# Optimization experiments

Hardware: AMD Instinct MI355X
Metric: run time of the kernel (lower is better)

The kernel has to match this reference:

```python
import jax, jax.numpy as jnp
import numpy as np

N, E, F, T, H = 100000, 3_200_000, 64, 12, 32


def _lin(k, fin, fout):
    s = 1.0 / np.sqrt(fin)
    k1, k2 = jax.random.split(k)
    W = jax.random.uniform(k1, (fin, fout), jnp.float32, -s, s)
    b = jax.random.uniform(k2, (fout,), jnp.float32, -s, s)
    return W, b


def _lstm_w(k, fin):
    s = 1.0 / np.sqrt(H)
    k1, k2, k3, k4 = jax.random.split(k, 4)
    return (jax.random.uniform(k1, (4 * H, fin), jnp.float32, -s, s),
            jax.random.uniform(k2, (4 * H, H), jnp.float32, -s, s),
            jax.random.uniform(k3, (4 * H,), jnp.float32, -s, s),
            jax.random.uniform(k4, (4 * H,), jnp.float32, -s, s))


def setup_inputs() -> dict:
    key = jax.random.key(0)
    ks = jax.random.split(key, 12)
    x = jax.random.normal(ks[0], (N, F), jnp.float32)
    edge_index = jax.random.randint(ks[1], (2, E), 0, N, dtype=jnp.int32)
    W_fp, b_fp = _lin(ks[2], F, 64)
    W_g1, b_g1 = _lin(ks[3], 64, 64)
    W_g2, b_g2 = _lin(ks[4], 64, 32)
    W_g3, b_g3 = _lin(ks[5], 32, 16)
    W_tp, b_tp = _lin(ks[6], 1, 16)
    Wih0, Whh0, bih0, bhh0 = _lstm_w(ks[7], 16)
    Wih1, Whh1, bih1, bhh1 = _lstm_w(ks[8], H)
    W_fc1, b_fc1 = _lin(ks[9], H, 16)
    W_fc2, b_fc2 = _lin(ks[10], 16, 1)
    return dict(x=x, edge_index=edge_index, W_fp=W_fp, b_fp=b_fp,
                W_g1=W_g1, b_g1=b_g1, W_g2=W_g2, b_g2=b_g2, W_g3=W_g3, b_g3=b_g3,
                W_tp=W_tp, b_tp=b_tp,
                Wih0=Wih0, Whh0=Whh0, bih0=bih0, bhh0=bhh0,
                Wih1=Wih1, Whh1=Whh1, bih1=bih1, bhh1=bhh1,
                W_fc1=W_fc1, b_fc1=b_fc1, W_fc2=W_fc2, b_fc2=b_fc2)


def reference(x, edge_index, W_fp, b_fp, W_g1, b_g1, W_g2, b_g2, W_g3, b_g3,
              W_tp, b_tp, Wih0, Whh0, bih0, bhh0, Wih1, Whh1, bih1, bhh1,
              W_fc1, b_fc1, W_fc2, b_fc2):
    n = x.shape[0]
    loops = jnp.arange(n, dtype=edge_index.dtype)
    src = jnp.concatenate([edge_index[0], loops])  # self-loops, PyG GCNConv default
    dst = jnp.concatenate([edge_index[1], loops])
    deg = jax.ops.segment_sum(jnp.ones_like(src, dtype=x.dtype), dst, num_segments=n)
    dis = deg ** -0.5  # deg >= 1 because of self-loops
    norm = dis[src] * dis[dst]  # [E+N]

    def gcn(h, W, b):
        h = h @ W  # transform then propagate (PyG order)
        agg = jax.ops.segment_sum(h[src] * norm[:, None], dst, num_segments=n)
        return agg + b

    h = jax.nn.relu(x @ W_fp + b_fp)
    h = jax.nn.relu(gcn(h, W_g1, b_g1))        # dropout inactive (eval mode)
    h = jax.nn.relu(gcn(h, W_g2, b_g2))
    h_gcn = jax.nn.relu(gcn(h, W_g3, b_g3))    # NOTE: overwritten in original forward (dead)

    # temporal branch: last T raw features -> [N, T, 1] -> proj to 16
    t = x[:, -T:].reshape(n, T, 1) @ W_tp + b_tp  # [N, T, 16]

    def step(carry, xt):
        h0, c0, h1, c1 = carry
        g = xt @ Wih0.T + h0 @ Whh0.T + (bih0 + bhh0)
        i, f, gg, o = jnp.split(g, 4, axis=-1)  # torch gate order i,f,g,o
        c0 = jax.nn.sigmoid(f) * c0 + jax.nn.sigmoid(i) * jnp.tanh(gg)
        h0 = jax.nn.sigmoid(o) * jnp.tanh(c0)
        g = h0 @ Wih1.T + h1 @ Whh1.T + (bih1 + bhh1)
        i, f, gg, o = jnp.split(g, 4, axis=-1)
        c1 = jax.nn.sigmoid(f) * c1 + jax.nn.sigmoid(i) * jnp.tanh(gg)
        h1 = jax.nn.sigmoid(o) * jnp.tanh(c1)
        return (h0, c0, h1, c1), None

    z = jnp.zeros((n, H), x.dtype)
    (h0, c0, h1, c1), _ = jax.lax.scan(step, (z, z, z, z), jnp.swapaxes(t, 0, 1))
    out = jax.nn.relu(h1 @ W_fc1 + b_fc1) @ W_fc2 + b_fc2  # [N, 1]
    return out
```

## Files before the change

kernel.cpp:

```cpp
#include <hip/hip_runtime.h>


#define TSTEPS 12
#define BS 512
#define NPB (BS / 4)

__device__ __forceinline__ float fsig(float x) {
    float e = __expf(-x);
    return __builtin_amdgcn_rcpf(1.0f + e);
}

__device__ __forceinline__ float ftanh(float x) {
    float ax = fabsf(x);
    float e = __expf(-2.0f * ax);
    float r = (1.0f - e) * __builtin_amdgcn_rcpf(1.0f + e);
    return x < 0.0f ? -r : r;
}

__global__ void precomp_kernel(const float* __restrict__ Wih0,
                               const float* __restrict__ Wtp,
                               const float* __restrict__ btp,
                               const float* __restrict__ bih0,
                               const float* __restrict__ bhh0,
                               const float* __restrict__ bih1,
                               const float* __restrict__ bhh1,
                               float* __restrict__ ws) {
    int r = threadIdx.x;
    if (r < 128) {
        float a = 0.0f, c = 0.0f;
#pragma unroll
        for (int k = 0; k < 16; ++k) {
            float w = Wih0[r * 16 + k];
            a += w * Wtp[k];
            c += w * btp[k];
        }
        const int g4 = r >> 5;
        const int j  = r & 31;
        ws[j * 8 + g4]       = a;
        ws[j * 8 + 4 + g4]   = c + bih0[r] + bhh0[r];
        ws[256 + j * 4 + g4] = bih1[r] + bhh1[r];
    }
}

__device__ __forceinline__ float dot8(const float4 a0, const float4 a1,
                                      const float h[8]) {
    return a0.x*h[0] + a0.y*h[1] + a0.z*h[2] + a0.w*h[3]
         + a1.x*h[4] + a1.y*h[5] + a1.z*h[6] + a1.w*h[7];
}

__device__ __forceinline__ float rs4(float v0, float v1, float v2, float v3,
                                     bool hi2, bool hi1) {
    float sa = hi2 ? v0 : v2;
    float ka = hi2 ? v2 : v0;
    float sb = hi2 ? v1 : v3;
    float kb = hi2 ? v3 : v1;
    float u0 = ka + __shfl_xor(sa, 2);
    float u1 = kb + __shfl_xor(sb, 2);
    float sc = hi1 ? u0 : u1;
    float kc = hi1 ? u1 : u0;
    return kc + __shfl_xor(sc, 1);
}

__global__ __launch_bounds__(BS) void lstm_kernel(
    const float* __restrict__ x,
    const float* __restrict__ Whh0,
    const float* __restrict__ Wih1,
    const float* __restrict__ Whh1,
    const float* __restrict__ Wfc1,
    const float* __restrict__ bfc1,
    const float* __restrict__ Wfc2,
    const float* __restrict__ bfc2,
    const float* __restrict__ pre,
    float* __restrict__ out, int N)
{
    __shared__ __align__(16) float sW[12288];

    const int tid = threadIdx.x;
#pragma unroll
    for (int i = 0; i < 8; ++i) sW[i * BS + tid]        = Whh0[i * BS + tid];
#pragma unroll
    for (int i = 0; i < 8; ++i) sW[4096 + i * BS + tid] = Wih1[i * BS + tid];
#pragma unroll
    for (int i = 0; i < 8; ++i) sW[8192 + i * BS + tid] = Whh1[i * BS + tid];
    __syncthreads();

    const int s    = tid & 3;
    const int node = tid >> 2;
    const int so8  = s * 8;
    const bool hi2 = (s & 2) != 0;
    const bool hi1 = (s & 1) != 0;
    const int n  = blockIdx.x * NPB + node;
    const int nn = (n < N) ? n : (N > 0 ? N - 1 : 0);
    const float* xr = x + (size_t)nn * 64 + 52;

    float h0r[8], h1r[8], c0r[8], c1r[8], hn[8];
#pragma unroll
    for (int k = 0; k < 8; ++k) { h0r[k] = 0.0f; h1r[k] = 0.0f; c0r[k] = 0.0f; c1r[k] = 0.0f; }

#pragma unroll 1
    for (int t = 0; t < TSTEPS; ++t) {
        const float xval = xr[t];

#pragma unroll
        for (int jj = 0; jj < 8; ++jj) {
            const int jown = so8 + jj;
            float pI[4], pF[4], pG[4], pO[4];
#pragma unroll
            for (int g = 0; g < 4; ++g) {
                const int j = g * 8 + jj;
                const float* wi = &sW[(j      ) * 32 + so8];
                const float* wf = &sW[(j +  32) * 32 + so8];
                const float* wg = &sW[(j +  64) * 32 + so8];
                const float* wo = &sW[(j +  96) * 32 + so8];
                pI[g] = dot8(((const float4*)wi)[0], ((const float4*)wi)[1], h0r);
                pF[g] = dot8(((const float4*)wf)[0], ((const float4*)wf)[1], h0r);
                pG[g] = dot8(((const float4*)wg)[0], ((const float4*)wg)[1], h0r);
                pO[g] = dot8(((const float4*)wo)[0], ((const float4*)wo)[1], h0r);
                __builtin_amdgcn_sched_barrier(0);
            }
            const float SI = rs4(pI[0], pI[1], pI[2], pI[3], hi2, hi1);
            const float SF = rs4(pF[0], pF[1], pF[2], pF[3], hi2, hi1);
            const float SG = rs4(pG[0], pG[1], pG[2], pG[3], hi2, hi1);
            const float SO = rs4(pO[0], pO[1], pO[2], pO[3], hi2, hi1);
            const float4 pA = ((const float4*)pre)[jown * 2];
            const float4 pC = ((const float4*)pre)[jown * 2 + 1];
            const float gi = SI + pC.x + xval * pA.x;
            const float gf = SF + pC.y + xval * pA.y;
            const float gG = SG + pC.z + xval * pA.z;
            const float go = SO + pC.w + xval * pA.w;
            const float cc = fsig(gf) * c0r[jj] + fsig(gi) * ftanh(gG);
            c0r[jj] = cc;
            hn[jj]  = fsig(go) * ftanh(cc);
        }
#pragma unroll
        for (int k = 0; k < 8; ++k) h0r[k] = hn[k];

#pragma unroll
        for (int jj = 0; jj < 8; ++jj) {
            const int jown = so8 + jj;
            float pI[4], pF[4], pG[4], pO[4];
#pragma unroll
            for (int g = 0; g < 4; ++g) {
                const int j = g * 8 + jj;
                {
                    const float* ai = &sW[4096 + (j      ) * 32 + so8];
                    const float* af = &sW[4096 + (j +  32) * 32 + so8];
                    const float* ag = &sW[4096 + (j +  64) * 32 + so8];
                    const float* ao = &sW[4096 + (j +  96) * 32 + so8];
                    pI[g] = dot8(((const float4*)ai)[0], ((const float4*)ai)[1], h0r);
                    pF[g] = dot8(((const float4*)af)[0], ((const float4*)af)[1], h0r);
                    pG[g] = dot8(((const float4*)ag)[0], ((const float4*)ag)[1], h0r);
                    pO[g] = dot8(((const float4*)ao)[0], ((const float4*)ao)[1], h0r);
                }
                __builtin_amdgcn_sched_barrier(0);
                {
                    const float* bi = &sW[8192 + (j      ) * 32 + so8];
                    const float* bf = &sW[8192 + (j +  32) * 32 + so8];
                    const float* bg = &sW[8192 + (j +  64) * 32 + so8];
                    const float* bo = &sW[8192 + (j +  96) * 32 + so8];
                    pI[g] += dot8(((const float4*)bi)[0], ((const float4*)bi)[1], h1r);
                    pF[g] += dot8(((const float4*)bf)[0], ((const float4*)bf)[1], h1r);
                    pG[g] += dot8(((const float4*)bg)[0], ((const float4*)bg)[1], h1r);
                    pO[g] += dot8(((const float4*)bo)[0], ((const float4*)bo)[1], h1r);
                }
                __builtin_amdgcn_sched_barrier(0);
            }
            const float SI = rs4(pI[0], pI[1], pI[2], pI[3], hi2, hi1);
            const float SF = rs4(pF[0], pF[1], pF[2], pF[3], hi2, hi1);
            const float SG = rs4(pG[0], pG[1], pG[2], pG[3], hi2, hi1);
            const float SO = rs4(pO[0], pO[1], pO[2], pO[3], hi2, hi1);
            const float4 pD = ((const float4*)(pre + 256))[jown];
            const float gi = SI + pD.x;
            const float gf = SF + pD.y;
            const float gG = SG + pD.z;
            const float go = SO + pD.w;
            const float cc = fsig(gf) * c1r[jj] + fsig(gi) * ftanh(gG);
            c1r[jj] = cc;
            hn[jj]  = fsig(go) * ftanh(cc);
        }
#pragma unroll
        for (int k = 0; k < 8; ++k) h1r[k] = hn[k];
    }

    float am[16];
#pragma unroll
    for (int m = 0; m < 16; ++m) am[m] = 0.0f;
#pragma unroll 1
    for (int kk = 0; kk < 8; ++kk) {
        const float* row = Wfc1 + (size_t)(so8 + kk) * 16;
        const float4 r0 = ((const float4*)row)[0];
        const float4 r1 = ((const float4*)row)[1];
        const float4 r2 = ((const float4*)row)[2];
        const float4 r3 = ((const float4*)row)[3];
        const float hv = h1r[kk];
        am[ 0] += r0.x*hv; am[ 1] += r0.y*hv; am[ 2] += r0.z*hv; am[ 3] += r0.w*hv;
        am[ 4] += r1.x*hv; am[ 5] += r1.y*hv; am[ 6] += r1.z*hv; am[ 7] += r1.w*hv;
        am[ 8] += r2.x*hv; am[ 9] += r2.y*hv; am[10] += r2.z*hv; am[11] += r2.w*hv;
        am[12] += r3.x*hv; am[13] += r3.y*hv; am[14] += r3.z*hv; am[15] += r3.w*hv;
    }
    float acc = bfc2[0];
#pragma unroll
    for (int m = 0; m < 16; ++m) {
        float a = am[m];
        a += __shfl_xor(a, 1); a += __shfl_xor(a, 2);
        acc += fmaxf(a + bfc1[m], 0.0f) * Wfc2[m];
    }
    if (s == 0 && n < N) out[n] = acc;
}

extern "C" void kernel_launch(void* const* d_in, const int* in_sizes, int n_in,
                              void* d_out, int out_size, void* d_ws, size_t ws_size,
                              hipStream_t stream) {
    (void)n_in; (void)out_size; (void)ws_size;
    const float* x    = (const float*)d_in[0];
    const float* Wtp  = (const float*)d_in[10];
    const float* btp  = (const float*)d_in[11];
    const float* Wih0 = (const float*)d_in[12];
    const float* Whh0 = (const float*)d_in[13];
    const float* bih0 = (const float*)d_in[14];
    const float* bhh0 = (const float*)d_in[15];
    const float* Wih1 = (const float*)d_in[16];
    const float* Whh1 = (const float*)d_in[17];
    const float* bih1 = (const float*)d_in[18];
    const float* bhh1 = (const float*)d_in[19];
    const float* Wfc1 = (const float*)d_in[20];
    const float* bfc1 = (const float*)d_in[21];
    const float* Wfc2 = (const float*)d_in[22];
    const float* bfc2 = (const float*)d_in[23];

    float* out = (float*)d_out;
    float* pre = (float*)d_ws;

    const int N = in_sizes[0] / 64;

    precomp_kernel<<<1, 128, 0, stream>>>(Wih0, Wtp, btp, bih0, bhh0, bih1, bhh1, pre);
    lstm_kernel<<<(N + NPB - 1) / NPB, BS, 0, stream>>>(
        x, Whh0, Wih1, Whh1, Wfc1, bfc1, Wfc2, bfc2, pre, out, N);
}
```

Before: 1.262 ms.

## Spill LSTM cell state to LDS and regroup gate dot products

```diff
diff --git a/kernel.cpp b/kernel.cpp
--- a/kernel.cpp
+++ b/kernel.cpp
@@ -59,6 +59,47 @@
     float sc = hi1 ? u0 : u1;
     float kc = hi1 ? u1 : u0;
     return kc + __shfl_xor(sc, 1);
+}
+
+__device__ __forceinline__ void l0pair(const float* __restrict__ sW,
+                                       int jj, int so8, int offA, int offB,
+                                       const float h[8], bool hi2, bool hi1,
+                                       float& SA, float& SB) {
+    float4 a0[4], a1[4], b0[4], b1[4];
+#pragma unroll
+    for (int g = 0; g < 4; ++g) {
+        const float* wa = &sW[(g * 8 + jj + offA) * 32 + so8];
+        const float* wb = &sW[(g * 8 + jj + offB) * 32 + so8];
+        a0[g] = ((const float4*)wa)[0]; a1[g] = ((const float4*)wa)[1];
+        b0[g] = ((const float4*)wb)[0]; b1[g] = ((const float4*)wb)[1];
+    }
+    float pa[4], pb[4];
+#pragma unroll
+    for (int g = 0; g < 4; ++g) {
+        pa[g] = dot8(a0[g], a1[g], h);
+        pb[g] = dot8(b0[g], b1[g], h);
+    }
+    SA = rs4(pa[0], pa[1], pa[2], pa[3], hi2, hi1);
+    SB = rs4(pb[0], pb[1], pb[2], pb[3], hi2, hi1);
+}
+
+__device__ __forceinline__ float l1gate(const float* __restrict__ sW,
+                                        int jj, int so8, int off,
+                                        const float h0[8], const float h1[8],
+                                        bool hi2, bool hi1) {
+    float4 a0[4], a1[4], b0[4], b1[4];
+#pragma unroll
+    for (int g = 0; g < 4; ++g) {
+        const float* ax = &sW[4096 + (g * 8 + jj + off) * 32 + so8];
+        const float* bx = &sW[8192 + (g * 8 + jj + off) * 32 + so8];
+        a0[g] = ((const float4*)ax)[0]; a1[g] = ((const float4*)ax)[1];
+        b0[g] = ((const float4*)bx)[0]; b1[g] = ((const float4*)bx)[1];
+    }
+    float p[4];
+#pragma unroll
+    for (int g = 0; g < 4; ++g)
+        p[g] = dot8(a0[g], a1[g], h0) + dot8(b0[g], b1[g], h1);
+    return rs4(p[0], p[1], p[2], p[3], hi2, hi1);
 }
 
 __global__ __launch_bounds__(BS) void lstm_kernel(
@@ -74,6 +115,8 @@
     float* __restrict__ out, int N)
 {
     __shared__ __align__(16) float sW[12288];
+    __shared__ float sc0[8 * BS];
+    __shared__ float sc1[8 * BS];
 
     const int tid = threadIdx.x;
 #pragma unroll
@@ -82,6 +125,11 @@
     for (int i = 0; i < 8; ++i) sW[4096 + i * BS + tid] = Wih1[i * BS + tid];
 #pragma unroll
     for (int i = 0; i < 8; ++i) sW[8192 + i * BS + tid] = Whh1[i * BS + tid];
+#pragma unroll
+    for (int jj = 0; jj < 8; ++jj) {
+        sc0[jj * BS + tid] = 0.0f;
+        sc1[jj * BS + tid] = 0.0f;
+    }
     __syncthreads();
 
     const int s    = tid & 3;
@@ -93,9 +141,9 @@
     const int nn = (n < N) ? n : (N > 0 ? N - 1 : 0);
     const float* xr = x + (size_t)nn * 64 + 52;
 
-    float h0r[8], h1r[8], c0r[8], c1r[8], hn[8];
-#pragma unroll
-    for (int k = 0; k < 8; ++k) { h0r[k] = 0.0f; h1r[k] = 0.0f; c0r[k] = 0.0f; c1r[k] = 0.0f; }
+    float h0r[8], h1r[8], hn[8];
+#pragma unroll
+    for (int k = 0; k < 8; ++k) { h0r[k] = 0.0f; h1r[k] = 0.0f; }
 
 #pragma unroll 1
     for (int t = 0; t < TSTEPS; ++t) {
@@ -104,32 +152,20 @@
 #pragma unroll
         for (int jj = 0; jj < 8; ++jj) {
             const int jown = so8 + jj;
-            float pI[4], pF[4], pG[4], pO[4];
-#pragma unroll
-            for (int g = 0; g < 4; ++g) {
-                const int j = g * 8 + jj;
-                const float* wi = &sW[(j      ) * 32 + so8];
-                const float* wf = &sW[(j +  32) * 32 + so8];
-                const float* wg = &sW[(j +  64) * 32 + so8];
-                const float* wo = &sW[(j +  96) * 32 + so8];
-                pI[g] = dot8(((const float4*)wi)[0], ((const float4*)wi)[1], h0r);
-                pF[g] = dot8(((const float4*)wf)[0], ((const float4*)wf)[1], h0r);
-                pG[g] = dot8(((const float4*)wg)[0], ((const float4*)wg)[1], h0r);
-                pO[g] = dot8(((const float4*)wo)[0], ((const float4*)wo)[1], h0r);
-                __builtin_amdgcn_sched_barrier(0);
-            }
-            const float SI = rs4(pI[0], pI[1], pI[2], pI[3], hi2, hi1);
-            const float SF = rs4(pF[0], pF[1], pF[2], pF[3], hi2, hi1);
-            const float SG = rs4(pG[0], pG[1], pG[2], pG[3], hi2, hi1);
-            const float SO = rs4(pO[0], pO[1], pO[2], pO[3], hi2, hi1);
+            float SI, SF, SG, SO;
+            l0pair(sW, jj, so8,  0, 32, h0r, hi2, hi1, SI, SF);
+            __builtin_amdgcn_sched_barrier(0);
+            l0pair(sW, jj, so8, 64, 96, h0r, hi2, hi1, SG, SO);
+            __builtin_amdgcn_sched_barrier(0);
             const float4 pA = ((const float4*)pre)[jown * 2];
             const float4 pC = ((const float4*)pre)[jown * 2 + 1];
             const float gi = SI + pC.x + xval * pA.x;
             const float gf = SF + pC.y + xval * pA.y;
             const float gG = SG + pC.z + xval * pA.z;
             const float go = SO + pC.w + xval * pA.w;
-            const float cc = fsig(gf) * c0r[jj] + fsig(gi) * ftanh(gG);
-            c0r[jj] = cc;
+            const int ci = jj * BS + tid;
+            const float cc = fsig(gf) * sc0[ci] + fsig(gi) * ftanh(gG);
+            sc0[ci] = cc;
             hn[jj]  = fsig(go) * ftanh(cc);
         }
 #pragma unroll
@@ -138,44 +174,22 @@
 #pragma unroll
         for (int jj = 0; jj < 8; ++jj) {
             const int jown = so8 + jj;
-            float pI[4], pF[4], pG[4], pO[4];
-#pragma unroll
-            for (int g = 0; g < 4; ++g) {
-                const int j = g * 8 + jj;
-                {
-                    const float* ai = &sW[4096 + (j      ) * 32 + so8];
-                    const float* af = &sW[4096 + (j +  32) * 32 + so8];
-                    const float* ag = &sW[4096 + (j +  64) * 32 + so8];
-                    const float* ao = &sW[4096 + (j +  96) * 32 + so8];
-                    pI[g] = dot8(((const float4*)ai)[0], ((const float4*)ai)[1], h0r);
-                    pF[g] = dot8(((const float4*)af)[0], ((const float4*)af)[1], h0r);
-                    pG[g] = dot8(((const float4*)ag)[0], ((const float4*)ag)[1], h0r);
-                    pO[g] = dot8(((const float4*)ao)[0], ((const float4*)ao)[1], h0r);
-                }
-                __builtin_amdgcn_sched_barrier(0);
-                {
-                    const float* bi = &sW[8192 + (j      ) * 32 + so8];
-                    const float* bf = &sW[8192 + (j +  32) * 32 + so8];
-                    const float* bg = &sW[8192 + (j +  64) * 32 + so8];
-                    const float* bo = &sW[8192 + (j +  96) * 32 + so8];
-                    pI[g] += dot8(((const float4*)bi)[0], ((const float4*)bi)[1], h1r);
-                    pF[g] += dot8(((const float4*)bf)[0], ((const float4*)bf)[1], h1r);
-                    pG[g] += dot8(((const float4*)bg)[0], ((const float4*)bg)[1], h1r);
-                    pO[g] += dot8(((const float4*)bo)[0], ((const float4*)bo)[1], h1r);
-                }
-                __builtin_amdgcn_sched_barrier(0);
-            }
-            const float SI = rs4(pI[0], pI[1], pI[2], pI[3], hi2, hi1);
-            const float SF = rs4(pF[0], pF[1], pF[2], pF[3], hi2, hi1);
-            const float SG = rs4(pG[0], pG[1], pG[2], pG[3], hi2, hi1);
-            const float SO = rs4(pO[0], pO[1], pO[2], pO[3], hi2, hi1);
+            const float SI = l1gate(sW, jj, so8,  0, h0r, h1r, hi2, hi1);
+            __builtin_amdgcn_sched_barrier(0);
+            const float SF = l1gate(sW, jj, so8, 32, h0r, h1r, hi2, hi1);
+            __builtin_amdgcn_sched_barrier(0);
+            const float SG = l1gate(sW, jj, so8, 64, h0r, h1r, hi2, hi1);
+            __builtin_amdgcn_sched_barrier(0);
+            const float SO = l1gate(sW, jj, so8, 96, h0r, h1r, hi2, hi1);
+            __builtin_amdgcn_sched_barrier(0);
             const float4 pD = ((const float4*)(pre + 256))[jown];
             const float gi = SI + pD.x;
             const float gf = SF + pD.y;
             const float gG = SG + pD.z;
             const float go = SO + pD.w;
-            const float cc = fsig(gf) * c1r[jj] + fsig(gi) * ftanh(gG);
-            c1r[jj] = cc;
+            const int ci = jj * BS + tid;
+            const float cc = fsig(gf) * sc1[ci] + fsig(gi) * ftanh(gG);
+            sc1[ci] = cc;
             hn[jj]  = fsig(go) * ftanh(cc);
         }
 #pragma unroll
```

Result: no change. 1.241 ms (median of 2 runs) (-1.7%).
